# Optimization experiments

Measured on AMD Instinct MI355X. Metric: run time of the kernel, lower is better.

## Reference

```python
import jax, jax.numpy as jnp
import numpy as np

NUM_HEADS = 16
HEAD_DIM = 64  # hidden = 1024


def setup_inputs() -> dict:
    key = jax.random.key(0)
    k1, k2, k3 = jax.random.split(key, 3)
    B, S, Hd = 4, 4096, NUM_HEADS * HEAD_DIM
    x = jax.random.normal(k1, (B, S, Hd), dtype=jnp.float32)
    # xavier-uniform-ish scaling for the dense kernels
    Wqkv = jax.random.normal(k2, (Hd, 3 * Hd), dtype=jnp.float32) * (2.0 / (Hd + 3 * Hd)) ** 0.5
    bqkv = jnp.zeros((3 * Hd,), dtype=jnp.float32)
    Wout = jax.random.normal(k3, (Hd, Hd), dtype=jnp.float32) * (1.0 / Hd) ** 0.5
    bout = jnp.zeros((Hd,), dtype=jnp.float32)
    return {"x": x, "Wqkv": Wqkv, "bqkv": bqkv, "Wout": Wout, "bout": bout}


def reference(x, Wqkv, bqkv, Wout, bout):
    B, S, _ = x.shape
    H, D = NUM_HEADS, HEAD_DIM
    qkv = jnp.einsum('bsc,cf->bsf', x, Wqkv) + bqkv  # [B,S,3*H*D]
    q, k, v = jnp.split(qkv, 3, axis=-1)
    # source transposes to [B,H,S,D] before calling flax dot_product_attention_weights,
    # which interprets dims as [..., q_len=H, num_heads=S, depth=D]  (shape bug, kept faithfully)
    q = q.reshape(B, S, H, D).transpose(0, 2, 1, 3)  # [B,H,S,D]
    k = k.reshape(B, S, H, D).transpose(0, 2, 1, 3)
    v = v.reshape(B, S, H, D).transpose(0, 2, 1, 3)
    scale = D ** -0.5
    # flax: einsum('...qhd,...khd->...hqk') -> weights [B, S, H, H]
    logits = jnp.einsum('bqhd,bkhd->bhqk', q * scale, k)
    attn = jax.nn.softmax(logits, axis=-1)  # softmax over key-head axis
    # source: einsum('bhqk,bkhd->bqhd', weights, v) -> [B, H, S, D]
    out = jnp.einsum('bhqk,bkhd->bqhd', attn, v)
    out = out.transpose(0, 2, 1, 3).reshape(B, S, H * D)  # [B,S,hidden]
    return jnp.einsum('bsc,cf->bsf', out, Wout) + bout
```

## Files before the change

### kernel.cpp

```cpp
#include <hip/hip_runtime.h>
#include <hip/hip_bf16.h>

using bf16 = __hip_bfloat16;
typedef __bf16 bf16x8_t __attribute__((ext_vector_type(8)));
typedef float f32x4_t __attribute__((ext_vector_type(4)));

__device__ __forceinline__ void gl16(bf16* l, const bf16* g) {
  __builtin_amdgcn_global_load_lds(
      (const __attribute__((address_space(1))) unsigned int*)g,
      (__attribute__((address_space(3))) unsigned int*)l, 16, 0, 0);
}

#define BARRIER() do { asm volatile("" ::: "memory"); __builtin_amdgcn_s_barrier(); asm volatile("" ::: "memory"); } while (0)
#define WAITVM(N) asm volatile("s_waitcnt vmcnt(" #N ")" ::: "memory")

__global__ __launch_bounds__(256) void prep_fused(const float* __restrict__ x,
                                                  const float* __restrict__ Wqkv,
                                                  const float* __restrict__ Wout,
                                                  bf16* __restrict__ xb,
                                                  bf16* __restrict__ w1t,
                                                  bf16* __restrict__ w2t) {
  __shared__ float t[32][33];
  const int bid = blockIdx.x;
  if (bid < 16384) {
    int i = bid * 256 + threadIdx.x;
    float4 v = ((const float4*)x)[i];
    union { ushort4 u; bf16 b[4]; } o;
    o.b[0] = __float2bfloat16(v.x);
    o.b[1] = __float2bfloat16(v.y);
    o.b[2] = __float2bfloat16(v.z);
    o.b[3] = __float2bfloat16(v.w);
    ((ushort4*)xb)[i] = o.u;
    return;
  }
  const float* in; bf16* out; int R, C, gx, gy;
  if (bid < 16384 + 3072) {
    int idx = bid - 16384; in = Wqkv; out = w1t; R = 1024; C = 3072;
    gx = idx % 96; gy = idx / 96;
  } else {
    int idx = bid - 16384 - 3072; in = Wout; out = w2t; R = 1024; C = 1024;
    gx = idx & 31; gy = idx >> 5;
  }
  int bx = gx * 32, by = gy * 32;
  int tx = threadIdx.x & 31, ty = threadIdx.x >> 5;
#pragma unroll
  for (int r = 0; r < 32; r += 8)
    t[ty + r][tx] = in[(size_t)(by + ty + r) * C + bx + tx];
  __syncthreads();
#pragma unroll
  for (int r = 0; r < 32; r += 8)
    out[(size_t)(bx + ty + r) * R + by + tx] = __float2bfloat16(t[tx][ty + r]);
}


__device__ __forceinline__ void readA(const bf16* lb, int half, int wr, int lr, int lg, int exr,
                                      bf16x8_t (&af)[4][2]) {
  const bf16* ab = lb + half * 8192;
#pragma unroll
  for (int mi = 0; mi < 4; ++mi) {
    int R = wr * 64 + mi * 16 + lr;
    af[mi][0] = *(const bf16x8_t*)(ab + R * 64 + ((lg * 8) ^ exr));
    af[mi][1] = *(const bf16x8_t*)(ab + R * 64 + ((32 + lg * 8) ^ exr));
  }
}
__device__ __forceinline__ void readB(const bf16* lb, int half, int wc, int lr, int lg, int exr,
                                      bf16x8_t (&bfr)[2][2]) {
  const bf16* bb = lb + (2 + half) * 8192;
#pragma unroll
  for (int ni = 0; ni < 2; ++ni) {
    int R = wc * 32 + ni * 16 + lr;
    bfr[ni][0] = *(const bf16x8_t*)(bb + R * 64 + ((lg * 8) ^ exr));
    bfr[ni][1] = *(const bf16x8_t*)(bb + R * 64 + ((32 + lg * 8) ^ exr));
  }
}

template <int MH, int NH>
__device__ __forceinline__ void mfma16(bf16x8_t (&af)[4][2], bf16x8_t (&bfr)[2][2],
                                       f32x4_t (&acc)[8][4]) {
  __builtin_amdgcn_s_setprio(1);
#pragma unroll
  for (int mi = 0; mi < 4; ++mi)
#pragma unroll
    for (int ni = 0; ni < 2; ++ni) {
      f32x4_t& a = acc[MH * 4 + mi][NH * 2 + ni];
      a = __builtin_amdgcn_mfma_f32_16x16x32_bf16(af[mi][0], bfr[ni][0], a, 0, 0, 0);
      a = __builtin_amdgcn_mfma_f32_16x16x32_bf16(af[mi][1], bfr[ni][1], a, 0, 0, 0);
    }
  __builtin_amdgcn_s_setprio(0);
}

template <int OUT_BF16, int NWGX>
__global__ __launch_bounds__(512, 2) void gemm256p(const bf16* __restrict__ A,
                                                   const bf16* __restrict__ Bt,
                                                   const float* __restrict__ bias,
                                                   void* __restrict__ Cv) {
  constexpr int K = 1024;
  constexpr int N = NWGX * 256;
  constexpr int TT = NWGX / 4;
  constexpr int G = TT * 16;
  constexpr int CPX = NWGX * 8;

  __shared__ __align__(16) bf16 lds[65536];
  const int tid = threadIdx.x;
  const int bx = blockIdx.x;

  const int wid = tid >> 6, lane = tid & 63;
  const int wr = wid >> 2, wc = wid & 3;
  const int lr = lane & 15, lg = lane >> 4;
  const int exr = (lr & 7) << 3;

  const int srow = tid >> 3;
  const int colg = ((((tid & 7) * 16) ^ ((srow & 7) << 4)) >> 1);
  const int browc0 = (srow >> 5) * 64 + (srow & 31);

  auto tileMN = [&](int tt, int& m0, int& n0) {
    int orig = bx + (tt << 8);
    int swz = (orig & 7) * CPX + (orig >> 3);
    m0 = (swz / NWGX) * 256;
    n0 = (swz % NWGX) * 256;
  };

  auto stageA = [&](int g, int h) {
    if (g >= G) return;
    int m0, n0; tileMN(g >> 4, m0, n0);
    const bf16* g0 = A + (size_t)(m0 + h * 64 + srow) * K + (g & 15) * 64 + colg;
    bf16* l = lds + (g & 1) * 32768 + h * 8192 + tid * 8;
    gl16(l, g0); gl16(l + 4096, g0 + (size_t)128 * K);
  };
  auto stageB = [&](int g, int h) {
    if (g >= G) return;
    int m0, n0; tileMN(g >> 4, m0, n0);
    const bf16* g0 = Bt + (size_t)(n0 + browc0 + h * 32) * K + (g & 15) * 64 + colg;
    bf16* l = lds + (g & 1) * 32768 + (2 + h) * 8192 + tid * 8;
    gl16(l, g0); gl16(l + 4096, g0 + (size_t)128 * K);
  };

  f32x4_t acc[8][4] = {};
  bf16x8_t af1[4][2], af2[4][2], b0[2][2], b1[2][2];

  stageA(0, 0); stageB(0, 0); stageA(0, 1); stageB(0, 1);
  stageA(1, 0); stageB(1, 0);
  WAITVM(4);
  BARRIER();
  readA(lds, 0, wr, lr, lg, exr, af1);
  readB(lds, 0, wc, lr, lg, exr, b0);

  for (int g = 0; g < G; ++g) {
    const bf16* cb = lds + (g & 1) * 32768;
    const bf16* nb = lds + ((g & 1) ^ 1) * 32768;

    stageA(g + 1, 1);
    BARRIER();
    readB(cb, 1, wc, lr, lg, exr, b1);
    mfma16<0, 0>(af1, b0, acc);

    stageB(g + 1, 1);
    BARRIER();
    readA(cb, 1, wr, lr, lg, exr, af2);
    mfma16<0, 1>(af1, b1, acc);

    stageA(g + 2, 0);
    BARRIER();
    mfma16<1, 0>(af2, b0, acc);

    stageB(g + 2, 0);
    if (g < G - 2) { WAITVM(4); } else { WAITVM(0); }
    BARRIER();
    if (g < G - 1) {
      readA(nb, 0, wr, lr, lg, exr, af1);
      readB(nb, 0, wc, lr, lg, exr, b0);
    }
    mfma16<1, 1>(af2, b1, acc);

    if ((g & 15) == 15) {
      BARRIER();
      int m0, n0; tileMN(g >> 4, m0, n0);
      float bv[4];
#pragma unroll
      for (int n = 0; n < 4; ++n) bv[n] = bias[n0 + wc * 64 + n * 16 + lr];
#pragma unroll
      for (int m = 0; m < 8; ++m) {
        int row = m0 + wr * 128 + m * 16 + lg * 4;
#pragma unroll
        for (int j = 0; j < 4; ++j) {
#pragma unroll
          for (int n = 0; n < 4; ++n) {
            int col = n0 + wc * 64 + n * 16 + lr;
            float v = acc[m][n][j] + bv[n];
            if (OUT_BF16)
              ((bf16*)Cv)[(size_t)(row + j) * N + col] = __float2bfloat16(v);
            else
              ((float*)Cv)[(size_t)(row + j) * N + col] = v;
            acc[m][n][j] = 0.f;
          }
        }
      }
    }
  }
}

#define PSTR 48
__global__ __launch_bounds__(256) void attn_tok(const bf16* __restrict__ qkv,
                                                bf16* __restrict__ out) {
  __shared__ __align__(16) bf16 vs[4][1024];
  __shared__ __align__(16) bf16 ps[4][16 * PSTR];
  const int w = threadIdx.x >> 6, l = threadIdx.x & 63;
  const int t = blockIdx.x * 4 + w;
  const int lr = l & 15, lg = l >> 4;
  const bf16* base = qkv + (size_t)t * 3072;

  bf16x8_t v0 = *(const bf16x8_t*)(base + 2048 + l * 16);
  bf16x8_t v1 = *(const bf16x8_t*)(base + 2048 + l * 16 + 8);
  *(bf16x8_t*)(&vs[w][l * 16]) = v0;
  *(bf16x8_t*)(&vs[w][l * 16 + 8]) = v1;

  *(unsigned long long*)(&ps[w][(l >> 2) * PSTR + 16 + (l & 3) * 4]) = 0ULL;

  const bf16* qp = base + lr * 64 + lg * 8;
  const bf16* kp = base + 1024 + lr * 64 + lg * 8;
  bf16x8_t qa0 = *(const bf16x8_t*)qp;
  bf16x8_t ka0 = *(const bf16x8_t*)kp;
  bf16x8_t qa1 = *(const bf16x8_t*)(qp + 32);
  bf16x8_t ka1 = *(const bf16x8_t*)(kp + 32);
  f32x4_t s = {};
  s = __builtin_amdgcn_mfma_f32_16x16x32_bf16(qa0, ka0, s, 0, 0, 0);
  s = __builtin_amdgcn_mfma_f32_16x16x32_bf16(qa1, ka1, s, 0, 0, 0);

#pragma unroll
  for (int j = 0; j < 4; ++j) {
    float x = s[j] * 0.125f;
    float mx = x;
#pragma unroll
    for (int off = 8; off; off >>= 1) mx = fmaxf(mx, __shfl_xor(mx, off, 16));
    float e = __expf(x - mx);
    float sum = e;
#pragma unroll
    for (int off = 8; off; off >>= 1) sum += __shfl_xor(sum, off, 16);
    ps[w][(lg * 4 + j) * PSTR + lr] = __float2bfloat16(e / sum);
  }

  bf16x8_t pf = *(const bf16x8_t*)(&ps[w][lr * PSTR + lg * 8]);
  bf16x8_t vf[4] = {};
  if (l < 32) {
#pragma unroll
    for (int c = 0; c < 4; ++c)
#pragma unroll
      for (int j = 0; j < 8; ++j)
        vf[c][j] = (__bf16)vs[w][(lg * 8 + j) * 64 + c * 16 + lr];
  }
  f32x4_t o[4] = {};
#pragma unroll
  for (int c = 0; c < 4; ++c)
    o[c] = __builtin_amdgcn_mfma_f32_16x16x32_bf16(pf, vf[c], o[c], 0, 0, 0);

  bf16* ob = out + (size_t)t * 1024;
#pragma unroll
  for (int c = 0; c < 4; ++c)
#pragma unroll
    for (int j = 0; j < 4; ++j)
      ob[(lg * 4 + j) * 64 + c * 16 + lr] = __float2bfloat16(o[c][j]);
}

extern "C" void kernel_launch(void* const* d_in, const int* in_sizes, int n_in,
                              void* d_out, int out_size, void* d_ws, size_t ws_size,
                              hipStream_t stream) {
  const float* x    = (const float*)d_in[0];
  const float* Wqkv = (const float*)d_in[1];
  const float* bqkv = (const float*)d_in[2];
  const float* Wout = (const float*)d_in[3];
  const float* bout = (const float*)d_in[4];
  float* y = (float*)d_out;

  const int T = 16384, HD = 1024, N1 = 3072;

  char* ws = (char*)d_ws;
  size_t off = 0;
  bf16* xb  = (bf16*)(ws + off); off += (size_t)T * HD * 2;
  bf16* w1t = (bf16*)(ws + off); off += (size_t)N1 * HD * 2;
  bf16* w2t = (bf16*)(ws + off); off += (size_t)HD * HD * 2;
  bf16* qkv = (bf16*)(ws + off); off += (size_t)T * N1 * 2;
  if (ws_size < off) return;
  bf16* ao = xb;

  prep_fused<<<16384 + 3072 + 1024, 256, 0, stream>>>(x, Wqkv, Wout, xb, w1t, w2t);
  gemm256p<1, 12><<<256, 512, 0, stream>>>(xb, w1t, bqkv, qkv);
  attn_tok<<<T / 4, 256, 0, stream>>>(qkv, ao);
  gemm256p<0, 4><<<256, 512, 0, stream>>>(ao, w2t, bout, y);
}
```

Baseline: 199.8 us.

## Fuse fp32-to-bf16 conversion of x into the QKV GEMM A-operand load

Drops the separate elementwise pass that converted x to bf16 and wrote it to workspace. A new GEMM variant now loads fp32 A tiles into registers, converts them to bf16 and writes them to LDS itself, while B still streams through global_load_lds. This removes a full write and reread of the 32MB activation, but the GEMM now reads twice as many A bytes, and the register-staged loads may pipeline less well than the direct-to-LDS path.

```diff
diff --git a/kernel.cpp b/kernel.cpp
--- a/kernel.cpp
+++ b/kernel.cpp
@@ -13,32 +13,20 @@
 
 #define BARRIER() do { asm volatile("" ::: "memory"); __builtin_amdgcn_s_barrier(); asm volatile("" ::: "memory"); } while (0)
 #define WAITVM(N) asm volatile("s_waitcnt vmcnt(" #N ")" ::: "memory")
-
-__global__ __launch_bounds__(256) void prep_fused(const float* __restrict__ x,
-                                                  const float* __restrict__ Wqkv,
-                                                  const float* __restrict__ Wout,
-                                                  bf16* __restrict__ xb,
-                                                  bf16* __restrict__ w1t,
-                                                  bf16* __restrict__ w2t) {
+#define LGKM0() asm volatile("s_waitcnt lgkmcnt(0)" ::: "memory")
+
+__global__ __launch_bounds__(256) void prep_t(const float* __restrict__ Wqkv,
+                                              const float* __restrict__ Wout,
+                                              bf16* __restrict__ w1t,
+                                              bf16* __restrict__ w2t) {
   __shared__ float t[32][33];
   const int bid = blockIdx.x;
-  if (bid < 16384) {
-    int i = bid * 256 + threadIdx.x;
-    float4 v = ((const float4*)x)[i];
-    union { ushort4 u; bf16 b[4]; } o;
-    o.b[0] = __float2bfloat16(v.x);
-    o.b[1] = __float2bfloat16(v.y);
-    o.b[2] = __float2bfloat16(v.z);
-    o.b[3] = __float2bfloat16(v.w);
-    ((ushort4*)xb)[i] = o.u;
-    return;
-  }
   const float* in; bf16* out; int R, C, gx, gy;
-  if (bid < 16384 + 3072) {
-    int idx = bid - 16384; in = Wqkv; out = w1t; R = 1024; C = 3072;
-    gx = idx % 96; gy = idx / 96;
+  if (bid < 3072) {
+    in = Wqkv; out = w1t; R = 1024; C = 3072;
+    gx = bid % 96; gy = bid / 96;
   } else {
-    int idx = bid - 16384 - 3072; in = Wout; out = w2t; R = 1024; C = 1024;
+    int idx = bid - 3072; in = Wout; out = w2t; R = 1024; C = 1024;
     gx = idx & 31; gy = idx >> 5;
   }
   int bx = gx * 32, by = gy * 32;
@@ -51,7 +39,6 @@
   for (int r = 0; r < 32; r += 8)
     out[(size_t)(bx + ty + r) * R + by + tx] = __float2bfloat16(t[tx][ty + r]);
 }
-
 
 __device__ __forceinline__ void readA(const bf16* lb, int half, int wr, int lr, int lg, int exr,
                                       bf16x8_t (&af)[4][2]) {
@@ -87,6 +74,137 @@
       a = __builtin_amdgcn_mfma_f32_16x16x32_bf16(af[mi][1], bfr[ni][1], a, 0, 0, 0);
     }
   __builtin_amdgcn_s_setprio(0);
+}
+
+template <int NWGX>
+__global__ __launch_bounds__(512, 2) void gemm256f(const float* __restrict__ Af,
+                                                   const bf16* __restrict__ Bt,
+                                                   const float* __restrict__ bias,
+                                                   bf16* __restrict__ Cv) {
+  constexpr int K = 1024;
+  constexpr int N = NWGX * 256;
+  constexpr int TT = NWGX / 4;
+  constexpr int G = TT * 16;
+  constexpr int CPX = NWGX * 8;
+
+  __shared__ __align__(16) bf16 lds[65536];
+  const int tid = threadIdx.x;
+  const int bx = blockIdx.x;
+
+  const int wid = tid >> 6, lane = tid & 63;
+  const int wr = wid >> 2, wc = wid & 3;
+  const int lr = lane & 15, lg = lane >> 4;
+  const int exr = (lr & 7) << 3;
+
+  const int srow = tid >> 3;
+  const int colg = ((((tid & 7) * 16) ^ ((srow & 7) << 4)) >> 1);
+  const int browc0 = (srow >> 5) * 64 + (srow & 31);
+
+  auto tileMN = [&](int tt, int& m0, int& n0) {
+    int orig = bx + (tt << 8);
+    int swz = (orig & 7) * CPX + (orig >> 3);
+    m0 = (swz / NWGX) * 256;
+    n0 = (swz % NWGX) * 256;
+  };
+
+  float4 rA[4];
+  auto loadA = [&](int g, int h) {
+    if (g >= G) return;
+    int m0, n0; tileMN(g >> 4, m0, n0);
+    const float* s0 = Af + (size_t)(m0 + h * 64 + srow) * K + (g & 15) * 64 + colg;
+    const float* s1 = s0 + (size_t)128 * K;
+    rA[0] = *(const float4*)s0;
+    rA[1] = *(const float4*)(s0 + 4);
+    rA[2] = *(const float4*)s1;
+    rA[3] = *(const float4*)(s1 + 4);
+  };
+  auto writeA = [&](int g, int h) {
+    if (g >= G) return;
+    bf16* l = lds + (g & 1) * 32768 + h * 8192 + tid * 8;
+    union { float4 f4[2]; float f[8]; } u0, u1;
+    u0.f4[0] = rA[0]; u0.f4[1] = rA[1];
+    u1.f4[0] = rA[2]; u1.f4[1] = rA[3];
+    bf16x8_t v0, v1;
+#pragma unroll
+    for (int j = 0; j < 8; ++j) { v0[j] = (__bf16)u0.f[j]; v1[j] = (__bf16)u1.f[j]; }
+    *(bf16x8_t*)l = v0;
+    *(bf16x8_t*)(l + 4096) = v1;
+  };
+  auto stageB = [&](int g, int h) {
+    if (g >= G) return;
+    int m0, n0; tileMN(g >> 4, m0, n0);
+    const bf16* g0 = Bt + (size_t)(n0 + browc0 + h * 32) * K + (g & 15) * 64 + colg;
+    bf16* l = lds + (g & 1) * 32768 + (2 + h) * 8192 + tid * 8;
+    gl16(l, g0); gl16(l + 4096, g0 + (size_t)128 * K);
+  };
+
+  f32x4_t acc[8][4] = {};
+  bf16x8_t af1[4][2], af2[4][2], b0[2][2], b1[2][2];
+
+  loadA(0, 0);
+  stageB(0, 0); stageB(0, 1);
+  writeA(0, 0);
+  loadA(0, 1);
+  writeA(0, 1);
+  loadA(1, 0);
+  stageB(1, 0);
+  WAITVM(6);
+  LGKM0();
+  BARRIER();
+  readA(lds, 0, wr, lr, lg, exr, af1);
+  readB(lds, 0, wc, lr, lg, exr, b0);
+
+  for (int g = 0; g < G; ++g) {
+    const bf16* cb = lds + (g & 1) * 32768;
+    const bf16* nb = lds + ((g & 1) ^ 1) * 32768;
+
+    writeA(g + 1, 0);
+    loadA(g + 1, 1);
+    BARRIER();
+    readB(cb, 1, wc, lr, lg, exr, b1);
+    mfma16<0, 0>(af1, b0, acc);
+
+    stageB(g + 1, 1);
+    BARRIER();
+    readA(cb, 1, wr, lr, lg, exr, af2);
+    mfma16<0, 1>(af1, b1, acc);
+
+    writeA(g + 1, 1);
+    loadA(g + 2, 0);
+    BARRIER();
+    mfma16<1, 0>(af2, b0, acc);
+
+    stageB(g + 2, 0);
+    if (g < G - 2) { WAITVM(6); } else { WAITVM(0); }
+    LGKM0();
+    BARRIER();
+    if (g < G - 1) {
+      readA(nb, 0, wr, lr, lg, exr, af1);
+      readB(nb, 0, wc, lr, lg, exr, b0);
+    }
+    mfma16<1, 1>(af2, b1, acc);
+
+    if ((g & 15) == 15) {
+      BARRIER();
+      int m0, n0; tileMN(g >> 4, m0, n0);
+      float bv[4];
+#pragma unroll
+      for (int n = 0; n < 4; ++n) bv[n] = bias[n0 + wc * 64 + n * 16 + lr];
+#pragma unroll
+      for (int m = 0; m < 8; ++m) {
+        int row = m0 + wr * 128 + m * 16 + lg * 4;
+#pragma unroll
+        for (int j = 0; j < 4; ++j) {
+#pragma unroll
+          for (int n = 0; n < 4; ++n) {
+            int col = n0 + wc * 64 + n * 16 + lr;
+            Cv[(size_t)(row + j) * N + col] = __float2bfloat16(acc[m][n][j] + bv[n]);
+            acc[m][n][j] = 0.f;
+          }
+        }
+      }
+    }
+  }
 }
 
 template <int OUT_BF16, int NWGX>
@@ -275,15 +393,14 @@
 
   char* ws = (char*)d_ws;
   size_t off = 0;
-  bf16* xb  = (bf16*)(ws + off); off += (size_t)T * HD * 2;
+  bf16* ao  = (bf16*)(ws + off); off += (size_t)T * HD * 2;
   bf16* w1t = (bf16*)(ws + off); off += (size_t)N1 * HD * 2;
   bf16* w2t = (bf16*)(ws + off); off += (size_t)HD * HD * 2;
   bf16* qkv = (bf16*)(ws + off); off += (size_t)T * N1 * 2;
   if (ws_size < off) return;
-  bf16* ao = xb;
-
-  prep_fused<<<16384 + 3072 + 1024, 256, 0, stream>>>(x, Wqkv, Wout, xb, w1t, w2t);
-  gemm256p<1, 12><<<256, 512, 0, stream>>>(xb, w1t, bqkv, qkv);
+
+  prep_t<<<3072 + 1024, 256, 0, stream>>>(Wqkv, Wout, w1t, w2t);
+  gemm256f<12><<<256, 512, 0, stream>>>(x, w1t, bqkv, qkv);
   attn_tok<<<T / 4, 256, 0, stream>>>(qkv, ao);
   gemm256p<0, 4><<<256, 512, 0, stream>>>(ao, w2t, bout, y);
 }
```

Measured after the change: 312.2 us. +56.3%, slower.
